# Kernel tuning notes

Measured on AMD Instinct MI355X. Metric: run time of the kernel, lower is better.

Reference implementation:

```python
import jax, jax.numpy as jnp
import numpy as np

EPS = 1e-5

def _ln(x, g, b):
    m = jnp.mean(x, axis=-1, keepdims=True)
    v = jnp.var(x, axis=-1, keepdims=True)
    return (x - m) * jax.lax.rsqrt(v + EPS) * g + b

def _gelu(x):
    return jax.nn.gelu(x, approximate=False)  # torch nn.GELU default is exact erf

def setup_inputs() -> dict:
    key = jax.random.key(0)
    B, N, D, H = 4, 1024, 128, 12
    HID = H * D
    ks = jax.random.split(key, 16)
    s = lambda k, sh, fan: jax.random.normal(k, sh, jnp.float32) * (fan ** -0.5)
    return {
        "x": jax.random.normal(ks[0], (B, N, D), jnp.float32),
        # project: LN(D) -> Linear(D,HID) -> GELU -> Linear(HID,HID)
        "ln1_g": jnp.ones((D,), jnp.float32), "ln1_b": jnp.zeros((D,), jnp.float32),
        "W1": s(ks[1], (D, HID), D), "b1": jnp.zeros((HID,), jnp.float32),
        "W2": s(ks[2], (HID, HID), HID), "b2": jnp.zeros((HID,), jnp.float32),
        # shared Attention(inc=D, outc=D)
        "aln_g": jnp.ones((D,), jnp.float32), "aln_b": jnp.zeros((D,), jnp.float32),
        "Wqkv": s(ks[3], (D, 3 * D), D), "bqkv": jnp.zeros((3 * D,), jnp.float32),
        "Wl": s(ks[4], (D, D), D), "bl": jnp.zeros((D,), jnp.float32),
        # out_proj: LN(HID) -> Linear(HID, D) -> GELU
        "lno_g": jnp.ones((HID,), jnp.float32), "lno_b": jnp.zeros((HID,), jnp.float32),
        "Wo": s(ks[5], (HID, D), HID), "bo": jnp.zeros((D,), jnp.float32),
    }

def reference(x, ln1_g, ln1_b, W1, b1, W2, b2,
              aln_g, aln_b, Wqkv, bqkv, Wl, bl,
              lno_g, lno_b, Wo, bo):
    B, N, D = x.shape
    # project (dropout is identity in eval mode)
    h = _ln(x, ln1_g, ln1_b)
    h = _gelu(h @ W1 + b1)
    h = h @ W2 + b2                      # [B, N, H*D]
    H = h.shape[-1] // D
    # chunk along last dim into H features of width D; fold heads into batch
    f = h.reshape(B, N, H, D).transpose(0, 2, 1, 3).reshape(B * H, N, D)
    # shared Attention applied to each head-chunk
    a = _ln(f, aln_g, aln_b)
    qkv = a @ Wqkv + bqkv
    q, k, v = jnp.split(qkv, 3, axis=-1)
    scores = jax.nn.softmax(jnp.einsum('bnd,bmd->bnm', q, k) * (D ** -0.5), axis=-1)
    o = jnp.einsum('bnm,bmd->bnd', scores, v)
    o = o @ Wl + bl
    o = _gelu(o + f)                     # [B*H, N, D]
    # concat heads back along last dim
    feats = o.reshape(B, H, N, D).transpose(0, 2, 1, 3).reshape(B, N, H * D)
    out = _gelu(_ln(feats, lno_g, lno_b) @ Wo + bo)
    return out
```

## Files before the change

### kernel.cpp

```cpp
#include <hip/hip_runtime.h>
#include <stdint.h>

typedef unsigned short u16;
typedef __attribute__((ext_vector_type(8))) short short8;
typedef __attribute__((ext_vector_type(4))) float floatx4;

__device__ inline float b2f(u16 u) {
  union { uint32_t i; float f; } x; x.i = ((uint32_t)u) << 16; return x.f;
}
__device__ inline u16 f2b(float f) {
  union { float f; uint32_t i; } x; x.f = f;
  uint32_t r = (x.i + 0x7FFFu + ((x.i >> 16) & 1u)) >> 16;
  return (u16)r;
}
__device__ inline float gelu_f(float v) {
  return 0.5f * v * (1.0f + erff(v * 0.70710678118654752440f));
}

#define MFMA16(a, b, c) __builtin_amdgcn_mfma_f32_16x16x32_bf16((a), (b), (c), 0, 0, 0)

__device__ __forceinline__ void gl2lds16(const u16* g, u16* l) {
  __builtin_amdgcn_global_load_lds(
      (const __attribute__((address_space(1))) uint32_t*)(uintptr_t)g,
      (__attribute__((address_space(3))) uint32_t*)(uint32_t)(uintptr_t)l,
      16, 0, 0);
}

__global__ __launch_bounds__(256)
void tpose_all_kernel(const float* __restrict__ W1, const float* __restrict__ W2,
                      const float* __restrict__ Wqkv, const float* __restrict__ Wl,
                      const float* __restrict__ Wo,
                      u16* __restrict__ w1t, u16* __restrict__ w2t,
                      u16* __restrict__ wqkvt, u16* __restrict__ wlt,
                      u16* __restrict__ wot) {
  int id = blockIdx.x;
  const float* src; u16* dst; int R, C, bx, by;
  if (id < 2304)      { src = W2;   dst = w2t;   R = 1536; C = 1536; bx = (id % 48) * 32; by = (id / 48) * 32; }
  else if (id < 2496) { id -= 2304; src = W1;   dst = w1t;   R = 128;  C = 1536; bx = (id % 48) * 32; by = (id / 48) * 32; }
  else if (id < 2688) { id -= 2496; src = Wo;   dst = wot;   R = 1536; C = 128;  bx = (id % 4) * 32;  by = (id / 4) * 32; }
  else if (id < 2736) { id -= 2688; src = Wqkv; dst = wqkvt; R = 128;  C = 384;  bx = (id % 12) * 32; by = (id / 12) * 32; }
  else                { id -= 2736; src = Wl;   dst = wlt;   R = 128;  C = 128;  bx = (id % 4) * 32;  by = (id / 4) * 32; }
  __shared__ u16 t[32][33];
  int tx = threadIdx.x & 31, ty = threadIdx.x >> 5;
  for (int i = 0; i < 32; i += 8)
    t[ty + i][tx] = f2b(src[(size_t)(by + ty + i) * C + bx + tx]);
  __syncthreads();
  for (int i = 0; i < 32; i += 8)
    dst[(size_t)(bx + ty + i) * R + by + tx] = t[tx][ty + i];
}

__global__ __launch_bounds__(256)
void ln128_f32_kernel(const float* __restrict__ X, const float* __restrict__ g,
                      const float* __restrict__ bb, u16* __restrict__ Y) {
  int tid = threadIdx.x, w = tid >> 6, lane = tid & 63;
  int row = blockIdx.x * 4 + w;
  const float* xr = X + (size_t)row * 128;
  float2 xv = *(const float2*)(xr + lane * 2);
  float x0 = xv.x, x1 = xv.y;
  float s = x0 + x1, s2 = x0 * x0 + x1 * x1;
  for (int m = 1; m < 64; m <<= 1) { s += __shfl_xor(s, m, 64); s2 += __shfl_xor(s2, m, 64); }
  float mean = s * (1.0f / 128.0f);
  float var = s2 * (1.0f / 128.0f) - mean * mean;
  float rstd = 1.0f / sqrtf(var + 1e-5f);
  float2 gv = *(const float2*)(g + lane * 2);
  float2 bv = *(const float2*)(bb + lane * 2);
  float y0 = (x0 - mean) * rstd * gv.x + bv.x;
  float y1 = (x1 - mean) * rstd * gv.y + bv.y;
  *(uint32_t*)(Y + (size_t)row * 128 + lane * 2) =
      (uint32_t)f2b(y0) | ((uint32_t)f2b(y1) << 16);
}

__global__ __launch_bounds__(256)
void ln128_perm_kernel(const u16* __restrict__ X, const float* __restrict__ g,
                       const float* __restrict__ bb, u16* __restrict__ Y) {
  int tid = threadIdx.x, w = tid >> 6, lane = tid & 63;
  int rid = blockIdx.x * 4 + w;
  int bh = rid >> 10, n = rid & 1023;
  int b = bh / 12, h = bh % 12;
  const u16* xr = X + ((size_t)(b * 1024 + n)) * 1536 + h * 128;
  uint32_t u = *(const uint32_t*)(xr + lane * 2);
  float x0 = b2f(u & 0xffff), x1 = b2f(u >> 16);
  float s = x0 + x1, s2 = x0 * x0 + x1 * x1;
  for (int m = 1; m < 64; m <<= 1) { s += __shfl_xor(s, m, 64); s2 += __shfl_xor(s2, m, 64); }
  float mean = s * (1.0f / 128.0f);
  float var = s2 * (1.0f / 128.0f) - mean * mean;
  float rstd = 1.0f / sqrtf(var + 1e-5f);
  float2 gv = *(const float2*)(g + lane * 2);
  float2 bv = *(const float2*)(bb + lane * 2);
  float y0 = (x0 - mean) * rstd * gv.x + bv.x;
  float y1 = (x1 - mean) * rstd * gv.y + bv.y;
  *(uint32_t*)(Y + (size_t)rid * 128 + lane * 2) =
      (uint32_t)f2b(y0) | ((uint32_t)f2b(y1) << 16);
}

__global__ __launch_bounds__(256)
void ln1536_kernel(const u16* __restrict__ X, const float* __restrict__ g,
                   const float* __restrict__ bb, u16* __restrict__ Y) {
  int row = blockIdx.x, tid = threadIdx.x;
  const u16* xr = X + (size_t)row * 1536;
  uint32_t u0 = *(const uint32_t*)(xr + tid * 6);
  uint32_t u1 = *(const uint32_t*)(xr + tid * 6 + 2);
  uint32_t u2 = *(const uint32_t*)(xr + tid * 6 + 4);
  float v[6] = { b2f(u0 & 0xffff), b2f(u0 >> 16), b2f(u1 & 0xffff),
                 b2f(u1 >> 16),    b2f(u2 & 0xffff), b2f(u2 >> 16) };
  float s = 0.f, s2 = 0.f;
  for (int j = 0; j < 6; j++) { s += v[j]; s2 += v[j] * v[j]; }
  for (int m = 1; m < 64; m <<= 1) { s += __shfl_xor(s, m, 64); s2 += __shfl_xor(s2, m, 64); }
  __shared__ float red[8];
  int w = tid >> 6, lane = tid & 63;
  if (lane == 0) { red[w] = s; red[4 + w] = s2; }
  __syncthreads();
  s = red[0] + red[1] + red[2] + red[3];
  s2 = red[4] + red[5] + red[6] + red[7];
  float mean = s * (1.0f / 1536.0f);
  float var = s2 * (1.0f / 1536.0f) - mean * mean;
  float rstd = 1.0f / sqrtf(var + 1e-5f);
  uint32_t o[3];
  for (int p = 0; p < 3; p++) {
    int c = tid * 6 + p * 2;
    float y0 = (v[p * 2] - mean) * rstd * g[c] + bb[c];
    float y1 = (v[p * 2 + 1] - mean) * rstd * g[c + 1] + bb[c + 1];
    o[p] = (uint32_t)f2b(y0) | ((uint32_t)f2b(y1) << 16);
  }
  u16* yr = Y + (size_t)row * 1536 + tid * 6;
  *(uint32_t*)(yr) = o[0];
  *(uint32_t*)(yr + 2) = o[1];
  *(uint32_t*)(yr + 4) = o[2];
}

__global__ __launch_bounds__(256)
void qkv_kernel(const u16* __restrict__ A, const u16* __restrict__ BT,
                const float* __restrict__ bias, u16* __restrict__ qkv,
                u16* __restrict__ vT) {
  const int K = 128;
  __shared__ __align__(16) u16 abuf[2 * 128 * 32];
  __shared__ __align__(16) u16 bbuf[2 * 128 * 32];
  int tid = threadIdx.x;
  int w = tid >> 6, lane = tid & 63, ln = lane & 15, quad = lane >> 4;
  int bm = blockIdx.x * 128, bn = blockIdx.y * 128;
  int wr = w >> 1, wc = w & 1;
  floatx4 acc[4][4] = {};
  auto STAGE = [&](int k0, int buf) {
    u16* ab = abuf + buf * 4096;
    u16* bb = bbuf + buf * 4096;
    for (int rd = 0; rd < 2; rd++) {
      int c = tid + rd * 256;
      int row = c >> 2, col = (c & 3) * 8;
      gl2lds16(A + (size_t)(bm + row) * K + k0 + col, ab + c * 8);
      gl2lds16(BT + (size_t)(bn + row) * K + k0 + col, bb + c * 8);
    }
  };
  STAGE(0, 0);
  int it = 0;
  for (int k0 = 0; k0 < K; k0 += 32, it++) {
    __syncthreads();
    if (k0 + 32 < K) STAGE(k0 + 32, (it + 1) & 1);
    const u16* ab = abuf + (it & 1) * 4096;
    const u16* bb = bbuf + (it & 1) * 4096;
    short8 af[4], bf[4];
    for (int i = 0; i < 4; i++)
      af[i] = *(const short8*)(ab + (wr * 64 + i * 16 + ln) * 32 + quad * 8);
    for (int j = 0; j < 4; j++)
      bf[j] = *(const short8*)(bb + (wc * 64 + j * 16 + ln) * 32 + quad * 8);
    for (int i = 0; i < 4; i++)
      for (int j = 0; j < 4; j++)
        acc[i][j] = MFMA16(af[i], bf[j], acc[i][j]);
  }
  if (blockIdx.y < 2) {
    const float QSCALE = 0.08838834764831845f * 1.4426950408889634f;
    float scale = (blockIdx.y == 0) ? QSCALE : 1.0f;
    for (int i = 0; i < 4; i++) {
      int row0 = bm + wr * 64 + i * 16 + quad * 4;
      for (int j = 0; j < 4; j++) {
        int col = bn + wc * 64 + j * 16 + ln;
        float bv = bias[col];
        for (int r = 0; r < 4; r++)
          qkv[(size_t)(row0 + r) * 256 + col] = f2b((acc[i][j][r] + bv) * scale);
      }
    }
  } else {
    int bh = bm >> 10;
    int nb = bm & 1023;
    u16* vp = vT + (size_t)bh * 128 * 1024;
    for (int i = 0; i < 4; i++) {
      int n0 = nb + wr * 64 + i * 16 + quad * 4;
      int npos = (n0 & ~31) | (((n0 >> 2) & 3) * 8) | (((n0 >> 4) & 1) * 4);
      for (int j = 0; j < 4; j++) {
        int d = wc * 64 + j * 16 + ln;
        float bv = bias[256 + d];
        u16 tmp[4];
        for (int r = 0; r < 4; r++) tmp[r] = f2b(acc[i][j][r] + bv);
        *(uint2*)(vp + (size_t)d * 1024 + npos) = *(const uint2*)tmp;
      }
    }
  }
}

template <int GELU, int RES, typename OUTT>
__global__ __launch_bounds__(256)
void gemm64_kernel(const u16* __restrict__ A, const u16* __restrict__ BT,
                   const float* __restrict__ bias, const u16* __restrict__ res,
                   OUTT* __restrict__ C, int M, int N, int K) {
  __shared__ __align__(16) u16 abuf[2 * 64 * 32];
  __shared__ __align__(16) u16 bbuf[2 * 128 * 32];
  int tid = threadIdx.x;
  int w = tid >> 6, lane = tid & 63, ln = lane & 15, quad = lane >> 4;
  int bm = blockIdx.x * 64, bn = blockIdx.y * 128;
  floatx4 acc[4][2] = {};
  auto STAGE = [&](int k0, int buf) {
    u16* ab = abuf + buf * 2048;
    u16* bb = bbuf + buf * 4096;
    for (int rd = 0; rd < 2; rd++) {
      int c = tid + rd * 256;
      int row = c >> 2, col = (c & 3) * 8;
      gl2lds16(BT + (size_t)(bn + row) * K + k0 + col, bb + c * 8);
    }
    {
      int c = tid;
      int row = c >> 2, col = (c & 3) * 8;
      gl2lds16(A + (size_t)(bm + row) * K + k0 + col, ab + c * 8);
    }
  };
  STAGE(0, 0);
  int it = 0;
  for (int k0 = 0; k0 < K; k0 += 32, it++) {
    __syncthreads();
    if (k0 + 32 < K) STAGE(k0 + 32, (it + 1) & 1);
    const u16* ab = abuf + (it & 1) * 2048;
    const u16* bb = bbuf + (it & 1) * 4096;
    short8 af[4], bf[2];
    for (int i = 0; i < 4; i++)
      af[i] = *(const short8*)(ab + (i * 16 + ln) * 32 + quad * 8);
    for (int j = 0; j < 2; j++)
      bf[j] = *(const short8*)(bb + (w * 32 + j * 16 + ln) * 32 + quad * 8);
    for (int i = 0; i < 4; i++)
      for (int j = 0; j < 2; j++)
        acc[i][j] = MFMA16(af[i], bf[j], acc[i][j]);
  }
  for (int i = 0; i < 4; i++) {
    int row0 = bm + i * 16 + quad * 4;
    for (int j = 0; j < 2; j++) {
      int col = bn + w * 32 + j * 16 + ln;
      float bv = bias[col];
      for (int r = 0; r < 4; r++) {
        float v = acc[i][j][r] + bv;
        if (RES) v += b2f(res[(size_t)(row0 + r) * N + col]);
        if (GELU) v = gelu_f(v);
        if constexpr (sizeof(OUTT) == 2)
          C[(size_t)(row0 + r) * N + col] = f2b(v);
        else
          C[(size_t)(row0 + r) * N + col] = v;
      }
    }
  }
}

template <int GELU, int RES, typename OUTT>
__global__ __launch_bounds__(256)
void gemm64b_kernel(const u16* __restrict__ A, const u16* __restrict__ BT,
                    const float* __restrict__ bias, const u16* __restrict__ res,
                    OUTT* __restrict__ C, int M, int N, int K) {
  __shared__ __align__(16) u16 abuf[2 * 2 * 64 * 32];
  __shared__ __align__(16) u16 bbuf[2 * 2 * 128 * 32];
  int tid = threadIdx.x;
  int w = tid >> 6, lane = tid & 63, ln = lane & 15, quad = lane >> 4;
  int bm = blockIdx.x * 64, bn = blockIdx.y * 128;
  floatx4 acc[4][2] = {};
  auto STAGE = [&](int k0, int buf) {
    u16* ab = abuf + buf * 4096;
    u16* bb = bbuf + buf * 8192;
    for (int ks = 0; ks < 2; ks++) {
      {
        int c = tid;
        int row = c >> 2, cc = c & 3;
        gl2lds16(A + (size_t)(bm + row) * K + k0 + ks * 32 + cc * 8,
                 ab + ks * 2048 + c * 8);
      }
      for (int rd = 0; rd < 2; rd++) {
        int c = tid + rd * 256;
        int row = c >> 2, cc = c & 3;
        gl2lds16(BT + (size_t)(bn + row) * K + k0 + ks * 32 + cc * 8,
                 bb + ks * 4096 + c * 8);
      }
    }
  };
  STAGE(0, 0);
  int it = 0;
  for (int k0 = 0; k0 < K; k0 += 64, it++) {
    __syncthreads();
    if (k0 + 64 < K) STAGE(k0 + 64, (it + 1) & 1);
    const u16* ab = abuf + (it & 1) * 4096;
    const u16* bb = bbuf + (it & 1) * 8192;
    short8 af[2][4], bf[2][2];
    for (int ks = 0; ks < 2; ks++) {
      for (int i = 0; i < 4; i++)
        af[ks][i] = *(const short8*)(ab + ks * 2048 + (i * 16 + ln) * 32 + quad * 8);
      for (int j = 0; j < 2; j++)
        bf[ks][j] = *(const short8*)(bb + ks * 4096 + (w * 32 + j * 16 + ln) * 32 + quad * 8);
    }
    for (int i = 0; i < 4; i++)
      for (int j = 0; j < 2; j++) {
        acc[i][j] = MFMA16(af[0][i], bf[0][j], acc[i][j]);
        acc[i][j] = MFMA16(af[1][i], bf[1][j], acc[i][j]);
      }
  }
  for (int i = 0; i < 4; i++) {
    int row0 = bm + i * 16 + quad * 4;
    for (int j = 0; j < 2; j++) {
      int col = bn + w * 32 + j * 16 + ln;
      float bv = bias[col];
      for (int r = 0; r < 4; r++) {
        float v = acc[i][j][r] + bv;
        if (RES) v += b2f(res[(size_t)(row0 + r) * N + col]);
        if (GELU) v = gelu_f(v);
        if constexpr (sizeof(OUTT) == 2)
          C[(size_t)(row0 + r) * N + col] = f2b(v);
        else
          C[(size_t)(row0 + r) * N + col] = v;
      }
    }
  }
}

__global__ __launch_bounds__(256)
void gemmwl_kernel(const u16* __restrict__ A, const u16* __restrict__ BT,
                   const float* __restrict__ bias, const u16* __restrict__ res,
                   u16* __restrict__ feats) {
  const int K = 128;
  __shared__ __align__(16) u16 abuf[64 * 32];
  __shared__ __align__(16) u16 bbuf[128 * 32];
  int tid = threadIdx.x;
  int w = tid >> 6, lane = tid & 63, ln = lane & 15, quad = lane >> 4;
  int bm = blockIdx.x * 64;
  floatx4 acc[4][2] = {};
  for (int k0 = 0; k0 < K; k0 += 32) {
    __syncthreads();
    for (int rd = 0; rd < 2; rd++) {
      int c = tid + rd * 256;
      int row = c >> 2, col = (c & 3) * 8;
      gl2lds16(BT + (size_t)row * K + k0 + col, bbuf + c * 8);
    }
    {
      int c = tid;
      int row = c >> 2, col = (c & 3) * 8;
      gl2lds16(A + (size_t)(bm + row) * K + k0 + col, abuf + c * 8);
    }
    __syncthreads();
    short8 af[4], bf[2];
    for (int i = 0; i < 4; i++)
      af[i] = *(const short8*)(abuf + (i * 16 + ln) * 32 + quad * 8);
    for (int j = 0; j < 2; j++)
      bf[j] = *(const short8*)(bbuf + (w * 32 + j * 16 + ln) * 32 + quad * 8);
    for (int i = 0; i < 4; i++)
      for (int j = 0; j < 2; j++)
        acc[i][j] = MFMA16(af[i], bf[j], acc[i][j]);
  }
  int bh = bm >> 10, nb = bm & 1023;
  int b = bh / 12, hh = bh % 12;
  size_t obase = ((size_t)b * 1024) * 1536 + hh * 128;
  for (int i = 0; i < 4; i++) {
    int n0 = nb + i * 16 + quad * 4;
    for (int j = 0; j < 2; j++) {
      int col = w * 32 + j * 16 + ln;
      float bv = bias[col];
      for (int r = 0; r < 4; r++) {
        size_t idx = obase + (size_t)(n0 + r) * 1536 + col;
        float v = acc[i][j][r] + bv + b2f(res[idx]);
        feats[idx] = f2b(gelu_f(v));
      }
    }
  }
}

__global__ __launch_bounds__(256)
void gemm64_part_kernel(const u16* __restrict__ A, const u16* __restrict__ BT,
                        float* __restrict__ pws, int Kfull, int kspan) {
  __shared__ __align__(16) u16 abuf[2 * 64 * 32];
  __shared__ __align__(16) u16 bbuf[2 * 128 * 32];
  int tid = threadIdx.x;
  int w = tid >> 6, lane = tid & 63, ln = lane & 15, quad = lane >> 4;
  int bm = blockIdx.x * 64;
  int kbeg = blockIdx.y * kspan, kend = kbeg + kspan;
  float* Cp = pws + (size_t)blockIdx.y * 4096 * 128;
  floatx4 acc[4][2] = {};
  auto STAGE = [&](int k0, int buf) {
    u16* ab = abuf + buf * 2048;
    u16* bb = bbuf + buf * 4096;
    for (int rd = 0; rd < 2; rd++) {
      int c = tid + rd * 256;
      int row = c >> 2, col = (c & 3) * 8;
      gl2lds16(BT + (size_t)row * Kfull + k0 + col, bb + c * 8);
    }
    {
      int c = tid;
      int row = c >> 2, col = (c & 3) * 8;
      gl2lds16(A + (size_t)(bm + row) * Kfull + k0 + col, ab + c * 8);
    }
  };
  STAGE(kbeg, 0);
  int it = 0;
  for (int k0 = kbeg; k0 < kend; k0 += 32, it++) {
    __syncthreads();
    if (k0 + 32 < kend) STAGE(k0 + 32, (it + 1) & 1);
    const u16* ab = abuf + (it & 1) * 2048;
    const u16* bb = bbuf + (it & 1) * 4096;
    short8 af[4], bf[2];
    for (int i = 0; i < 4; i++)
      af[i] = *(const short8*)(ab + (i * 16 + ln) * 32 + quad * 8);
    for (int j = 0; j < 2; j++)
      bf[j] = *(const short8*)(bb + (w * 32 + j * 16 + ln) * 32 + quad * 8);
    for (int i = 0; i < 4; i++)
      for (int j = 0; j < 2; j++)
        acc[i][j] = MFMA16(af[i], bf[j], acc[i][j]);
  }
  for (int i = 0; i < 4; i++) {
    int row0 = bm + i * 16 + quad * 4;
    for (int j = 0; j < 2; j++) {
      int col = w * 32 + j * 16 + ln;
      for (int r = 0; r < 4; r++)
        Cp[(size_t)(row0 + r) * 128 + col] = acc[i][j][r];
    }
  }
}

__global__ __launch_bounds__(256)
void combine_wo_kernel(const float* __restrict__ p, const float* __restrict__ bias,
                       float* __restrict__ out) {
  int i = blockIdx.x * 256 + threadIdx.x;
  const int SZ = 4096 * 128;
  float v = p[i] + p[i + SZ] + p[i + 2 * SZ] + p[i + 3 * SZ] + bias[i & 127];
  out[i] = gelu_f(v);
}

__global__ __launch_bounds__(256, 3)
void attn_kernel(const u16* __restrict__ qkv, const u16* __restrict__ vT,
                 u16* __restrict__ obuf) {
  int blk = blockIdx.x;
  int xcd = blk & 7, slot = blk >> 3;
  int bh = xcd * 6 + (slot >> 4);
  int qt = slot & 15;
  int tid = threadIdx.x, w = tid >> 6, lane = tid & 63, ln = lane & 15, quad = lane >> 4;
  int pair = w & 1, half = w >> 1;
  __shared__ __align__(16) u16 smem[24576 + 128];
  u16* kbuf = smem;
  u16* vbufs = smem + 8192;
  const int rs = 256;
  size_t base = (size_t)bh * 1024 * 256;
  const u16* qp = qkv + base;
  const u16* kp = qkv + base + 128;
  const u16* vp = vT + (size_t)bh * 128 * 1024;

  short8 qf[2][4];
  for (int g = 0; g < 2; g++) {
    int qrow = qt * 64 + pair * 32 + g * 16 + ln;
    for (int st = 0; st < 4; st++)
      qf[g][st] = *(const short8*)(qp + (size_t)qrow * rs + st * 32 + quad * 8);
  }

  short8 onesA;
  {
    short v = (ln == 0) ? (short)0x3F80 : (short)0;
    for (int j = 0; j < 8; j++) onesA[j] = v;
  }

  floatx4 o[2][8] = {};
  floatx4 l9[2] = {};

  auto STAGE_K = [&](int kt) {
    for (int it = 0; it < 4; it++) {
      int c = it * 256 + tid;
      int st = c >> 8, key = (c >> 2) & 63, cc = c & 3;
      gl2lds16(kp + (size_t)(kt * 64 + key) * rs + st * 32 + cc * 8, kbuf + c * 8);
    }
  };
  auto STAGE_V = [&](int kt, int buf) {
    u16* vb = vbufs + buf * 8192;
    for (int it = 0; it < 4; it++) {
      int c = it * 256 + tid;
      int kf = c >> 9, d = (c >> 2) & 127, cc = c & 3;
      gl2lds16(vp + (size_t)d * 1024 + kt * 64 + kf * 32 + cc * 8, vb + c * 8);
    }
  };

  STAGE_K(0);
  STAGE_V(0, 0);

  for (int kt = 0; kt < 16; kt++) {
    __syncthreads();

    short8 kfr[2][4];
    for (int tt = 0; tt < 2; tt++)
      for (int st = 0; st < 4; st++)
        kfr[tt][st] = *(const short8*)(kbuf + st * 2048 +
                                       ((half * 2 + tt) * 16 + ln) * 32 + quad * 8);
    __syncthreads();

    if (kt < 15) {
      STAGE_K(kt + 1);
      STAGE_V(kt + 1, (kt + 1) & 1);
    }

    floatx4 s[2][2] = {};
    for (int tt = 0; tt < 2; tt++)
      for (int st = 0; st < 4; st++) {
        s[0][tt] = MFMA16(kfr[tt][st], qf[0][st], s[0][tt]);
        s[1][tt] = MFMA16(kfr[tt][st], qf[1][st], s[1][tt]);
      }

    short8 pfrag[2];
    for (int g = 0; g < 2; g++) {
      float p0[4], p1[4];
      for (int r = 0; r < 4; r++) {
        p0[r] = exp2f(s[g][0][r]);
        p1[r] = exp2f(s[g][1][r]);
      }
      uint32_t a0, a1, b0, b1;
      asm("v_cvt_pk_bf16_f32 %0, %1, %2" : "=v"(a0) : "v"(p0[0]), "v"(p0[1]));
      asm("v_cvt_pk_bf16_f32 %0, %1, %2" : "=v"(a1) : "v"(p0[2]), "v"(p0[3]));
      asm("v_cvt_pk_bf16_f32 %0, %1, %2" : "=v"(b0) : "v"(p1[0]), "v"(p1[1]));
      asm("v_cvt_pk_bf16_f32 %0, %1, %2" : "=v"(b1) : "v"(p1[2]), "v"(p1[3]));
      union { uint32_t u[4]; short8 v; } pu;
      pu.u[0] = a0; pu.u[1] = a1; pu.u[2] = b0; pu.u[3] = b1;
      pfrag[g] = pu.v;
    }

    l9[0] = MFMA16(onesA, pfrag[0], l9[0]);
    l9[1] = MFMA16(onesA, pfrag[1], l9[1]);

    const u16* vb = vbufs + (kt & 1) * 8192;
    for (int dt = 0; dt < 8; dt++) {
      short8 av = *(const short8*)(vb + half * 4096 + (dt * 16 + ln) * 32 + quad * 8);
      o[0][dt] = MFMA16(av, pfrag[0], o[0][dt]);
      o[1][dt] = MFMA16(av, pfrag[1], o[1][dt]);
    }
  }

  float lsum[2];
  lsum[0] = __shfl(l9[0][0], ln);
  lsum[1] = __shfl(l9[1][0], ln);

  __syncthreads();
  float* mbuf = (float*)smem;
  float* lbuf = (float*)(smem + 16384);
  if (half == 1) {
    float* mp = mbuf + pair * 4096;
    for (int g = 0; g < 2; g++)
      for (int dt = 0; dt < 8; dt++)
        for (int r = 0; r < 4; r++)
          mp[(dt * 16 + quad * 4 + r) * 32 + ((g * 16 + ln + quad * 8) & 31)] = o[g][dt][r];
    if (quad == 0) {
      lbuf[pair * 32 + ln] = lsum[0];
      lbuf[pair * 32 + 16 + ln] = lsum[1];
    }
  }
  __syncthreads();
  if (half == 0) {
    float* mp = mbuf + pair * 4096;
    for (int g = 0; g < 2; g++) {
      float lt = lsum[g] + lbuf[pair * 32 + g * 16 + ln];
      float inv = 1.0f / lt;
      int n = qt * 64 + pair * 32 + g * 16 + ln;
      size_t ob = ((size_t)bh * 1024 + n) * 128;
      for (int dt = 0; dt < 8; dt++) {
        u16 tmp[4];
        for (int r = 0; r < 4; r++)
          tmp[r] = f2b((o[g][dt][r] +
                        mp[(dt * 16 + quad * 4 + r) * 32 + ((g * 16 + ln + quad * 8) & 31)]) * inv);
        *(uint2*)(obuf + ob + dt * 16 + quad * 4) = *(const uint2*)tmp;
      }
    }
  }
}

extern "C" void kernel_launch(void* const* d_in, const int* in_sizes, int n_in,
                              void* d_out, int out_size, void* d_ws, size_t ws_size,
                              hipStream_t stream) {
  (void)in_sizes; (void)n_in; (void)out_size; (void)ws_size;
  const float* x    = (const float*)d_in[0];
  const float* ln1g = (const float*)d_in[1];
  const float* ln1b = (const float*)d_in[2];
  const float* W1   = (const float*)d_in[3];
  const float* b1   = (const float*)d_in[4];
  const float* W2   = (const float*)d_in[5];
  const float* b2   = (const float*)d_in[6];
  const float* alng = (const float*)d_in[7];
  const float* alnb = (const float*)d_in[8];
  const float* Wqkv = (const float*)d_in[9];
  const float* bqkv = (const float*)d_in[10];
  const float* Wl   = (const float*)d_in[11];
  const float* bl   = (const float*)d_in[12];
  const float* lnog = (const float*)d_in[13];
  const float* lnob = (const float*)d_in[14];
  const float* Wo   = (const float*)d_in[15];
  const float* bo   = (const float*)d_in[16];
  float* out = (float*)d_out;

  char* ws = (char*)d_ws;
  size_t off = 0;
  auto alloc = [&](size_t elems) { u16* p = (u16*)(ws + off); off += elems * sizeof(u16); return p; };
  u16* w1t   = alloc((size_t)1536 * 128);
  u16* w2t   = alloc((size_t)1536 * 1536);
  u16* wqkvt = alloc((size_t)384 * 128);
  u16* wlt   = alloc((size_t)128 * 128);
  u16* wot   = alloc((size_t)128 * 1536);
  u16* lnx   = alloc((size_t)4096 * 128);
  u16* h1    = alloc((size_t)4096 * 1536);
  u16* h2    = alloc((size_t)4096 * 1536);
  u16* aln   = alloc((size_t)49152 * 128);
  u16* qkv   = alloc((size_t)49152 * 256);
  u16* obuf  = alloc((size_t)49152 * 128);
  u16* vT = h1;
  u16* feats = aln;
  u16* lnf = qkv;
  float* pws = (float*)h1;

  dim3 T(256);
  tpose_all_kernel<<<dim3(2752), T, 0, stream>>>(W1, W2, Wqkv, Wl, Wo,
                                                 w1t, w2t, wqkvt, wlt, wot);
  ln128_f32_kernel<<<dim3(4096 / 4), T, 0, stream>>>(x, ln1g, ln1b, lnx);
  gemm64_kernel<1, 0, u16><<<dim3(4096 / 64, 1536 / 128), T, 0, stream>>>(
      lnx, w1t, b1, nullptr, h1, 4096, 1536, 128);
  gemm64b_kernel<0, 0, u16><<<dim3(4096 / 64, 1536 / 128), T, 0, stream>>>(
      h1, w2t, b2, nullptr, h2, 4096, 1536, 1536);
  ln128_perm_kernel<<<dim3(49152 / 4), T, 0, stream>>>(h2, alng, alnb, aln);
  qkv_kernel<<<dim3(49152 / 128, 3), T, 0, stream>>>(aln, wqkvt, bqkv, qkv, vT);
  attn_kernel<<<dim3(768), T, 0, stream>>>(qkv, vT, obuf);
  gemmwl_kernel<<<dim3(49152 / 64), T, 0, stream>>>(obuf, wlt, bl, h2, feats);
  ln1536_kernel<<<dim3(4096), T, 0, stream>>>(feats, lnog, lnob, lnf);
  gemm64_part_kernel<<<dim3(4096 / 64, 4), T, 0, stream>>>(lnf, wot, pws, 1536, 384);
  combine_wo_kernel<<<dim3(4096 * 128 / 256), T, 0, stream>>>(pws, bo, out);
}
```

Measured before the change: 239.8 us.

## Double-buffer Wl GEMM and attention K tiles, cut a barrier per iteration

The Wl projection GEMM now keeps two LDS buffers and prefetches the next K-slice while computing the current one, so it needs one barrier per step instead of two. In the attention kernel, K tiles are also double-buffered, which removes the register copy of K fragments and one __syncthreads per key tile. K fragments are now read from LDS just before each MFMA. The attention launch bound is raised from 3 to 4 blocks per CU. The price is that attention LDS per block grows to about 64 KB, which may lower the number of resident blocks rather than raise it. The tighter register budget may also cause spills.

```diff
diff --git a/kernel.cpp b/kernel.cpp
--- a/kernel.cpp
+++ b/kernel.cpp
@@ -327,30 +327,38 @@
                    const float* __restrict__ bias, const u16* __restrict__ res,
                    u16* __restrict__ feats) {
   const int K = 128;
-  __shared__ __align__(16) u16 abuf[64 * 32];
-  __shared__ __align__(16) u16 bbuf[128 * 32];
+  __shared__ __align__(16) u16 abuf[2 * 64 * 32];
+  __shared__ __align__(16) u16 bbuf[2 * 128 * 32];
   int tid = threadIdx.x;
   int w = tid >> 6, lane = tid & 63, ln = lane & 15, quad = lane >> 4;
   int bm = blockIdx.x * 64;
   floatx4 acc[4][2] = {};
-  for (int k0 = 0; k0 < K; k0 += 32) {
-    __syncthreads();
+  auto STAGE = [&](int k0, int buf) {
+    u16* ab = abuf + buf * 2048;
+    u16* bb = bbuf + buf * 4096;
     for (int rd = 0; rd < 2; rd++) {
       int c = tid + rd * 256;
       int row = c >> 2, col = (c & 3) * 8;
-      gl2lds16(BT + (size_t)row * K + k0 + col, bbuf + c * 8);
+      gl2lds16(BT + (size_t)row * K + k0 + col, bb + c * 8);
     }
     {
       int c = tid;
       int row = c >> 2, col = (c & 3) * 8;
-      gl2lds16(A + (size_t)(bm + row) * K + k0 + col, abuf + c * 8);
-    }
+      gl2lds16(A + (size_t)(bm + row) * K + k0 + col, ab + c * 8);
+    }
+  };
+  STAGE(0, 0);
+  int it = 0;
+  for (int k0 = 0; k0 < K; k0 += 32, it++) {
     __syncthreads();
+    if (k0 + 32 < K) STAGE(k0 + 32, (it + 1) & 1);
+    const u16* ab = abuf + (it & 1) * 2048;
+    const u16* bb = bbuf + (it & 1) * 4096;
     short8 af[4], bf[2];
     for (int i = 0; i < 4; i++)
-      af[i] = *(const short8*)(abuf + (i * 16 + ln) * 32 + quad * 8);
+      af[i] = *(const short8*)(ab + (i * 16 + ln) * 32 + quad * 8);
     for (int j = 0; j < 2; j++)
-      bf[j] = *(const short8*)(bbuf + (w * 32 + j * 16 + ln) * 32 + quad * 8);
+      bf[j] = *(const short8*)(bb + (w * 32 + j * 16 + ln) * 32 + quad * 8);
     for (int i = 0; i < 4; i++)
       for (int j = 0; j < 2; j++)
         acc[i][j] = MFMA16(af[i], bf[j], acc[i][j]);
@@ -432,7 +440,7 @@
   out[i] = gelu_f(v);
 }
 
-__global__ __launch_bounds__(256, 3)
+__global__ __launch_bounds__(256, 4)
 void attn_kernel(const u16* __restrict__ qkv, const u16* __restrict__ vT,
                  u16* __restrict__ obuf) {
   int blk = blockIdx.x;
@@ -441,9 +449,9 @@
   int qt = slot & 15;
   int tid = threadIdx.x, w = tid >> 6, lane = tid & 63, ln = lane & 15, quad = lane >> 4;
   int pair = w & 1, half = w >> 1;
-  __shared__ __align__(16) u16 smem[24576 + 128];
-  u16* kbuf = smem;
-  u16* vbufs = smem + 8192;
+  __shared__ __align__(16) u16 smem[32768 + 128];
+  u16* kbufs = smem;
+  u16* vbufs = smem + 16384;
   const int rs = 256;
   size_t base = (size_t)bh * 1024 * 256;
   const u16* qp = qkv + base;
@@ -466,11 +474,12 @@
   floatx4 o[2][8] = {};
   floatx4 l9[2] = {};
 
-  auto STAGE_K = [&](int kt) {
+  auto STAGE_K = [&](int kt, int buf) {
+    u16* kb = kbufs + buf * 8192;
     for (int it = 0; it < 4; it++) {
       int c = it * 256 + tid;
       int st = c >> 8, key = (c >> 2) & 63, cc = c & 3;
-      gl2lds16(kp + (size_t)(kt * 64 + key) * rs + st * 32 + cc * 8, kbuf + c * 8);
+      gl2lds16(kp + (size_t)(kt * 64 + key) * rs + st * 32 + cc * 8, kb + c * 8);
     }
   };
   auto STAGE_V = [&](int kt, int buf) {
@@ -482,29 +491,27 @@
     }
   };
 
-  STAGE_K(0);
+  STAGE_K(0, 0);
   STAGE_V(0, 0);
 
   for (int kt = 0; kt < 16; kt++) {
     __syncthreads();
 
-    short8 kfr[2][4];
-    for (int tt = 0; tt < 2; tt++)
-      for (int st = 0; st < 4; st++)
-        kfr[tt][st] = *(const short8*)(kbuf + st * 2048 +
-                                       ((half * 2 + tt) * 16 + ln) * 32 + quad * 8);
-    __syncthreads();
-
     if (kt < 15) {
-      STAGE_K(kt + 1);
+      STAGE_K(kt + 1, (kt + 1) & 1);
       STAGE_V(kt + 1, (kt + 1) & 1);
     }
+
+    const u16* kb = kbufs + (kt & 1) * 8192;
+    const u16* vb = vbufs + (kt & 1) * 8192;
 
     floatx4 s[2][2] = {};
     for (int tt = 0; tt < 2; tt++)
       for (int st = 0; st < 4; st++) {
-        s[0][tt] = MFMA16(kfr[tt][st], qf[0][st], s[0][tt]);
-        s[1][tt] = MFMA16(kfr[tt][st], qf[1][st], s[1][tt]);
+        short8 kv = *(const short8*)(kb + st * 2048 +
+                                     ((half * 2 + tt) * 16 + ln) * 32 + quad * 8);
+        s[0][tt] = MFMA16(kv, qf[0][st], s[0][tt]);
+        s[1][tt] = MFMA16(kv, qf[1][st], s[1][tt]);
       }
 
     short8 pfrag[2];
@@ -527,7 +534,6 @@
     l9[0] = MFMA16(onesA, pfrag[0], l9[0]);
     l9[1] = MFMA16(onesA, pfrag[1], l9[1]);
 
-    const u16* vb = vbufs + (kt & 1) * 8192;
     for (int dt = 0; dt < 8; dt++) {
       short8 av = *(const short8*)(vb + half * 4096 + (dt * 16 + ln) * 32 + quad * 8);
       o[0][dt] = MFMA16(av, pfrag[0], o[0][dt]);
@@ -541,7 +547,7 @@
 
   __syncthreads();
   float* mbuf = (float*)smem;
-  float* lbuf = (float*)(smem + 16384);
+  float* lbuf = (float*)(smem + 32768);
   if (half == 1) {
     float* mp = mbuf + pair * 4096;
     for (int g = 0; g < 2; g++)
```

New measurement: 242.5 us. Within noise of the previous version (+1.1%).

## Fuse Wl projection, residual and GELU into attention kernel epilogue

Applied to the files above, without the earlier changes.

Removes the separate gemmwl kernel and the obuf round trip through global memory. The attention output tile is normalised, packed to bf16 into shared memory, and multiplied by Wl inside the same block. Bias, residual and GELU are applied there and written straight into the head-concatenated feats layout. Wl is pre-transposed into a k-chunked, permuted layout so it can be copied into LDS directly. This adds LDS traffic and registers to the attention kernel, which may lower its occupancy, in exchange for one less launch and less memory traffic.

```diff
diff --git a/kernel.cpp b/kernel.cpp
--- a/kernel.cpp
+++ b/kernel.cpp
@@ -34,19 +34,25 @@
                       u16* __restrict__ wqkvt, u16* __restrict__ wlt,
                       u16* __restrict__ wot) {
   int id = blockIdx.x;
-  const float* src; u16* dst; int R, C, bx, by;
+  const float* src; u16* dst; int R, C, bx, by, kind = 0;
   if (id < 2304)      { src = W2;   dst = w2t;   R = 1536; C = 1536; bx = (id % 48) * 32; by = (id / 48) * 32; }
   else if (id < 2496) { id -= 2304; src = W1;   dst = w1t;   R = 128;  C = 1536; bx = (id % 48) * 32; by = (id / 48) * 32; }
   else if (id < 2688) { id -= 2496; src = Wo;   dst = wot;   R = 1536; C = 128;  bx = (id % 4) * 32;  by = (id / 4) * 32; }
   else if (id < 2736) { id -= 2688; src = Wqkv; dst = wqkvt; R = 128;  C = 384;  bx = (id % 12) * 32; by = (id / 12) * 32; }
-  else                { id -= 2736; src = Wl;   dst = wlt;   R = 128;  C = 128;  bx = (id % 4) * 32;  by = (id / 4) * 32; }
+  else                { id -= 2736; src = Wl;   dst = wlt;   R = 128;  C = 128;  bx = (id % 4) * 32;  by = (id / 4) * 32; kind = 1; }
   __shared__ u16 t[32][33];
   int tx = threadIdx.x & 31, ty = threadIdx.x >> 5;
   for (int i = 0; i < 32; i += 8)
     t[ty + i][tx] = f2b(src[(size_t)(by + ty + i) * C + bx + tx]);
   __syncthreads();
-  for (int i = 0; i < 32; i += 8)
-    dst[(size_t)(bx + ty + i) * R + by + tx] = t[tx][ty + i];
+  if (kind == 0) {
+    for (int i = 0; i < 32; i += 8)
+      dst[(size_t)(bx + ty + i) * R + by + tx] = t[tx][ty + i];
+  } else {
+    int sig = ((tx >> 2) & 3) * 8 + ((tx >> 4) & 1) * 4 + (tx & 3);
+    for (int i = 0; i < 32; i += 8)
+      dst[(size_t)(by >> 5) * 4096 + (size_t)(bx + ty + i) * 32 + sig] = t[tx][ty + i];
+  }
 }
 
 __global__ __launch_bounds__(256)
@@ -323,56 +329,6 @@
 }
 
 __global__ __launch_bounds__(256)
-void gemmwl_kernel(const u16* __restrict__ A, const u16* __restrict__ BT,
-                   const float* __restrict__ bias, const u16* __restrict__ res,
-                   u16* __restrict__ feats) {
-  const int K = 128;
-  __shared__ __align__(16) u16 abuf[64 * 32];
-  __shared__ __align__(16) u16 bbuf[128 * 32];
-  int tid = threadIdx.x;
-  int w = tid >> 6, lane = tid & 63, ln = lane & 15, quad = lane >> 4;
-  int bm = blockIdx.x * 64;
-  floatx4 acc[4][2] = {};
-  for (int k0 = 0; k0 < K; k0 += 32) {
-    __syncthreads();
-    for (int rd = 0; rd < 2; rd++) {
-      int c = tid + rd * 256;
-      int row = c >> 2, col = (c & 3) * 8;
-      gl2lds16(BT + (size_t)row * K + k0 + col, bbuf + c * 8);
-    }
-    {
-      int c = tid;
-      int row = c >> 2, col = (c & 3) * 8;
-      gl2lds16(A + (size_t)(bm + row) * K + k0 + col, abuf + c * 8);
-    }
-    __syncthreads();
-    short8 af[4], bf[2];
-    for (int i = 0; i < 4; i++)
-      af[i] = *(const short8*)(abuf + (i * 16 + ln) * 32 + quad * 8);
-    for (int j = 0; j < 2; j++)
-      bf[j] = *(const short8*)(bbuf + (w * 32 + j * 16 + ln) * 32 + quad * 8);
-    for (int i = 0; i < 4; i++)
-      for (int j = 0; j < 2; j++)
-        acc[i][j] = MFMA16(af[i], bf[j], acc[i][j]);
-  }
-  int bh = bm >> 10, nb = bm & 1023;
-  int b = bh / 12, hh = bh % 12;
-  size_t obase = ((size_t)b * 1024) * 1536 + hh * 128;
-  for (int i = 0; i < 4; i++) {
-    int n0 = nb + i * 16 + quad * 4;
-    for (int j = 0; j < 2; j++) {
-      int col = w * 32 + j * 16 + ln;
-      float bv = bias[col];
-      for (int r = 0; r < 4; r++) {
-        size_t idx = obase + (size_t)(n0 + r) * 1536 + col;
-        float v = acc[i][j][r] + bv + b2f(res[idx]);
-        feats[idx] = f2b(gelu_f(v));
-      }
-    }
-  }
-}
-
-__global__ __launch_bounds__(256)
 void gemm64_part_kernel(const u16* __restrict__ A, const u16* __restrict__ BT,
                         float* __restrict__ pws, int Kfull, int kspan) {
   __shared__ __align__(16) u16 abuf[2 * 64 * 32];
@@ -434,7 +390,8 @@
 
 __global__ __launch_bounds__(256, 3)
 void attn_kernel(const u16* __restrict__ qkv, const u16* __restrict__ vT,
-                 u16* __restrict__ obuf) {
+                 const u16* __restrict__ wlt, const float* __restrict__ blp,
+                 const u16* __restrict__ h2res, u16* __restrict__ feats) {
   int blk = blockIdx.x;
   int xcd = blk & 7, slot = blk >> 3;
   int bh = xcd * 6 + (slot >> 4);
@@ -542,6 +499,7 @@
   __syncthreads();
   float* mbuf = (float*)smem;
   float* lbuf = (float*)(smem + 16384);
+  u16* obf = smem + 16512;
   if (half == 1) {
     float* mp = mbuf + pair * 4096;
     for (int g = 0; g < 2; g++)
@@ -559,15 +517,53 @@
     for (int g = 0; g < 2; g++) {
       float lt = lsum[g] + lbuf[pair * 32 + g * 16 + ln];
       float inv = 1.0f / lt;
-      int n = qt * 64 + pair * 32 + g * 16 + ln;
-      size_t ob = ((size_t)bh * 1024 + n) * 128;
+      int q = pair * 32 + g * 16 + ln;
       for (int dt = 0; dt < 8; dt++) {
-        u16 tmp[4];
+        float vv[4];
         for (int r = 0; r < 4; r++)
-          tmp[r] = f2b((o[g][dt][r] +
-                        mp[(dt * 16 + quad * 4 + r) * 32 + ((g * 16 + ln + quad * 8) & 31)]) * inv);
-        *(uint2*)(obuf + ob + dt * 16 + quad * 4) = *(const uint2*)tmp;
-      }
+          vv[r] = (o[g][dt][r] +
+                   mp[(dt * 16 + quad * 4 + r) * 32 + ((g * 16 + ln + quad * 8) & 31)]) * inv;
+        uint32_t w0, w1;
+        asm("v_cvt_pk_bf16_f32 %0, %1, %2" : "=v"(w0) : "v"(vv[0]), "v"(vv[1]));
+        asm("v_cvt_pk_bf16_f32 %0, %1, %2" : "=v"(w1) : "v"(vv[2]), "v"(vv[3]));
+        uint2 pk; pk.x = w0; pk.y = w1;
+        *(uint2*)(obf + (dt >> 1) * 2048 + q * 32 + quad * 8 + (dt & 1) * 4) = pk;
+      }
+    }
+  }
+  __syncthreads();
+  for (int rdi = 0; rdi < 8; rdi++) {
+    int c = rdi * 256 + tid;
+    gl2lds16(wlt + c * 8, smem + c * 8);
+  }
+  __syncthreads();
+
+  int b = bh / 12, hh = bh % 12;
+  size_t obase = ((size_t)b * 1024) * 1536 + hh * 128;
+  floatx4 cc[2][4] = {};
+  for (int kk = 0; kk < 4; kk++) {
+    short8 bf[4];
+    for (int qg = 0; qg < 4; qg++)
+      bf[qg] = *(const short8*)(obf + kk * 2048 + (qg * 16 + ln) * 32 + quad * 8);
+    for (int t = 0; t < 2; t++) {
+      short8 af = *(const short8*)(smem + kk * 4096 + ((w * 2 + t) * 16 + ln) * 32 + quad * 8);
+      for (int qg = 0; qg < 4; qg++)
+        cc[t][qg] = MFMA16(af, bf[qg], cc[t][qg]);
+    }
+  }
+  for (int t = 0; t < 2; t++) {
+    int c0 = (w * 2 + t) * 16 + quad * 4;
+    for (int qg = 0; qg < 4; qg++) {
+      int n = qt * 64 + qg * 16 + ln;
+      size_t idx = obase + (size_t)n * 1536 + c0;
+      uint2 rv = *(const uint2*)(h2res + idx);
+      const u16* rvp = (const u16*)&rv;
+      u16 tmp[4];
+      for (int r = 0; r < 4; r++) {
+        float v = cc[t][qg][r] + blp[c0 + r] + b2f(rvp[r]);
+        tmp[r] = f2b(gelu_f(v));
+      }
+      *(uint2*)(feats + idx) = *(const uint2*)tmp;
     }
   }
 }
@@ -608,7 +604,6 @@
   u16* h2    = alloc((size_t)4096 * 1536);
   u16* aln   = alloc((size_t)49152 * 128);
   u16* qkv   = alloc((size_t)49152 * 256);
-  u16* obuf  = alloc((size_t)49152 * 128);
   u16* vT = h1;
   u16* feats = aln;
   u16* lnf = qkv;
@@ -624,8 +619,7 @@
       h1, w2t, b2, nullptr, h2, 4096, 1536, 1536);
   ln128_perm_kernel<<<dim3(49152 / 4), T, 0, stream>>>(h2, alng, alnb, aln);
   qkv_kernel<<<dim3(49152 / 128, 3), T, 0, stream>>>(aln, wqkvt, bqkv, qkv, vT);
-  attn_kernel<<<dim3(768), T, 0, stream>>>(qkv, vT, obuf);
-  gemmwl_kernel<<<dim3(49152 / 64), T, 0, stream>>>(obuf, wlt, bl, h2, feats);
+  attn_kernel<<<dim3(768), T, 0, stream>>>(qkv, vT, wlt, bl, h2, feats);
   ln1536_kernel<<<dim3(4096), T, 0, stream>>>(feats, lnog, lnob, lnf);
   gemm64_part_kernel<<<dim3(4096 / 64, 4), T, 0, stream>>>(lnf, wot, pws, 1536, 384);
   combine_wo_kernel<<<dim3(4096 * 128 / 256), T, 0, stream>>>(pws, bo, out);
```

New measurement: 227.2 us. 1.06x faster.
